# Performance work log

Measured on AMD Instinct MI355X. Metric: run time of the kernel, lower is better.

## Reference

```python
import jax, jax.numpy as jnp
import numpy as np

DIM = 512
A_HEADS = 8
C_HEADS = 4
DH = 64
EPS = 1e-5


def layer_norm(x, g, b):
    mu = jnp.mean(x, axis=-1, keepdims=True)
    var = jnp.var(x, axis=-1, keepdims=True)
    return (x - mu) * jax.lax.rsqrt(var + EPS) * g + b


def setup_inputs() -> dict:
    key = jax.random.key(0)
    ks = jax.random.split(key, 8)
    inner_a = A_HEADS * DH  # 512
    inner_c = C_HEADS * DH  # 256
    s = 0.02
    return {
        "x": jax.random.normal(ks[0], (4, 192, DIM), dtype=jnp.float32),
        # Attention branch params
        "ln1_g": jnp.ones((DIM,), jnp.float32),
        "ln1_b": jnp.zeros((DIM,), jnp.float32),
        "Wqkv": jax.random.normal(ks[1], (DIM, 3 * inner_a), jnp.float32) * s,
        "Wo": jax.random.normal(ks[2], (inner_a, DIM), jnp.float32) * s,
        "bo": jnp.zeros((DIM,), jnp.float32),
        # Trittention branch params
        "ln2_g": jnp.ones((DIM,), jnp.float32),
        "ln2_b": jnp.zeros((DIM,), jnp.float32),
        "Wabcde": jax.random.normal(ks[3], (DIM, 5 * inner_c), jnp.float32) * s,
        "babcde": jnp.zeros((5 * inner_c,), jnp.float32),
        "Wp": jax.random.normal(ks[4], (inner_c, DIM), jnp.float32) * s,
        "bp": jnp.zeros((DIM,), jnp.float32),
    }


def _attention(x, ln_g, ln_b, Wqkv, Wo, bo):
    B, T, _ = x.shape
    xn = layer_norm(x, ln_g, ln_b)
    qkv = xn @ Wqkv  # [B,T,3*H*D]
    q, k, v = jnp.split(qkv, 3, axis=-1)
    def heads(t):
        return t.reshape(B, T, A_HEADS, DH).transpose(0, 2, 1, 3)  # [B,H,T,D]
    q, k, v = heads(q), heads(k), heads(v)
    scale = DH ** -0.5
    dots = jnp.einsum('bhqd,bhkd->bhqk', q, k) * scale
    attn = jax.nn.softmax(dots, axis=-1)
    out = jnp.einsum('bhqk,bhkd->bhqd', attn, v)
    out = out.transpose(0, 2, 1, 3).reshape(B, T, A_HEADS * DH)
    return out @ Wo + bo


def _trittention(x, ln_g, ln_b, Wabcde, babcde, Wp, bp):
    B, T, _ = x.shape
    xn = layer_norm(x, ln_g, ln_b)
    proj = xn @ Wabcde + babcde  # [B,T,5*H*D]
    a, b_, c, d_, e = jnp.split(proj, 5, axis=-1)
    def heads(t):
        return t.reshape(B, T, C_HEADS, DH)  # [B,T,H,D]
    a, b_, c, d_, e = heads(a), heads(b_), heads(c), heads(d_), heads(e)
    # cubic score: [B,H,S,T,Q]
    score = jnp.einsum('bshd,bthd,bqhd->bhstq', a, b_, c) / DH
    # softmax over joint (s,t) for each query q
    score = score.transpose(0, 1, 4, 2, 3).reshape(B, C_HEADS, T, T * T)
    attn = jax.nn.softmax(score, axis=-1).reshape(B, C_HEADS, T, T, T)
    z = (jnp.einsum('bhqst,bshd->bhqd', attn, d_)
         + jnp.einsum('bhqst,bthd->bhqd', attn, e))
    z = z.transpose(0, 2, 1, 3).reshape(B, T, C_HEADS * DH)
    return z @ Wp + bp


def reference(x, ln1_g, ln1_b, Wqkv, Wo, bo, ln2_g, ln2_b, Wabcde, babcde, Wp, bp):
    return (_attention(x, ln1_g, ln1_b, Wqkv, Wo, bo)
            + _trittention(x, ln2_g, ln2_b, Wabcde, babcde, Wp, bp))
```

## Files before the change

kernel.cpp:

```cpp
#include <hip/hip_runtime.h>
#include <cstdint>


#define B_   4
#define T_   192
#define DIM_ 512
#define AH   8
#define CH   4

typedef unsigned short u16;
typedef unsigned int   u32;
typedef __attribute__((ext_vector_type(8))) short short8;
typedef __attribute__((ext_vector_type(4))) float floatx4;
typedef __attribute__((ext_vector_type(4))) int intx4;
typedef __attribute__((ext_vector_type(2))) float f32x2;
typedef __attribute__((ext_vector_type(8))) _Float16 half8;
typedef __attribute__((ext_vector_type(2))) _Float16 half2v;
typedef __attribute__((ext_vector_type(2))) __fp16 fp16x2;

union Frag  { intx4 i; short8 s; };
union FragH { intx4 i; half8 h; };

__device__ __forceinline__ floatx4 mfma16(Frag a, Frag b, floatx4 c) {
    return __builtin_amdgcn_mfma_f32_16x16x32_bf16(a.s, b.s, c, 0, 0, 0);
}
__device__ __forceinline__ floatx4 mfma16h(FragH a, FragH b, floatx4 c) {
    return __builtin_amdgcn_mfma_f32_16x16x32_f16(a.h, b.h, c, 0, 0, 0);
}

__device__ __forceinline__ float fexp2(float x) {
    return __builtin_amdgcn_exp2f(x);
}

__device__ __forceinline__ float wave_reduce_sum(float v) {
#pragma unroll
    for (int off = 32; off >= 1; off >>= 1)
        v += __shfl_xor(v, off, 64);
    return v;
}

__device__ __forceinline__ u32 pack_rne(float x, float y) {
    u32 ux = __float_as_uint(x);
    u32 uy = __float_as_uint(y);
    ux += 0x7fffu + ((ux >> 16) & 1u);
    uy += 0x7fffu + ((uy >> 16) & 1u);
    return (ux >> 16) | (uy & 0xffff0000u);
}
__device__ __forceinline__ u16 bf16_rne(float x) {
    u32 u = __float_as_uint(x);
    u += 0x7fffu + ((u >> 16) & 1u);
    return (u16)(u >> 16);
}
__device__ __forceinline__ float bf16f(u16 h) { return __uint_as_float(((u32)h) << 16); }

__device__ __forceinline__ u32 pack_f16(float x, float y) {
    union { fp16x2 h; u32 u; } cv;
    cv.h = __builtin_amdgcn_cvt_pkrtz(x, y);
    return cv.u;
}
__device__ __forceinline__ u32 mul_h2(u32 a, u32 b) {
    union { u32 u; half2v h; } ua, ub, uw;
    ua.u = a; ub.u = b;
    uw.h = ua.h * ub.h;
    return uw.u;
}

__device__ __forceinline__ Frag ld_frag8(const u16* p) {
    Frag f;
    uint2 a = *(const uint2*)p;
    uint2 b = *(const uint2*)(p + 4);
    f.i = (intx4){ (int)a.x, (int)a.y, (int)b.x, (int)b.y };
    return f;
}

#define LOG2E 1.44269504088896f

__global__ __launch_bounds__(256) void prep_kernel(
    const float* __restrict__ x,
    const float* __restrict__ g1, const float* __restrict__ b1,
    const float* __restrict__ g2, const float* __restrict__ b2,
    u16* __restrict__ x1h, u16* __restrict__ x1l,
    u16* __restrict__ x2h, u16* __restrict__ x2l,
    const float* __restrict__ Wqkv, u16* __restrict__ wqh,
    const float* __restrict__ Wab,  u16* __restrict__ wah,
    const float* __restrict__ Wo,   const float* __restrict__ Wp,
    u16* __restrict__ wofh, u16* __restrict__ wofl)
{
    __shared__ union { float t[64][65]; float red[4][2]; } u;
    const int tid = threadIdx.x;
    if (blockIdx.x < 768) {
        int row = blockIdx.x;
        const float2 v = ((const float2*)(x + (size_t)row * DIM_))[tid];
        float s  = v.x + v.y;
        float s2 = v.x * v.x + v.y * v.y;
        s  = wave_reduce_sum(s);
        s2 = wave_reduce_sum(s2);
        int w = tid >> 6;
        if ((tid & 63) == 0) { u.red[w][0] = s; u.red[w][1] = s2; }
        __syncthreads();
        float ts  = u.red[0][0] + u.red[1][0] + u.red[2][0] + u.red[3][0];
        float ts2 = u.red[0][1] + u.red[1][1] + u.red[2][1] + u.red[3][1];
        float mean = ts * (1.0f / DIM_);
        float var  = ts2 * (1.0f / DIM_) - mean * mean;
        float rstd = rsqrtf(var + 1e-5f);
        int c0 = tid * 2;
        float n0 = (v.x - mean) * rstd;
        float n1 = (v.y - mean) * rstd;
        float a0 = n0 * g1[c0] + b1[c0], a1 = n1 * g1[c0 + 1] + b1[c0 + 1];
        float c2 = n0 * g2[c0] + b2[c0], c3 = n1 * g2[c0 + 1] + b2[c0 + 1];
        u16 h0 = bf16_rne(a0), h1 = bf16_rne(a1);
        u16 h2 = bf16_rne(c2), h3 = bf16_rne(c3);
        u16 l0 = bf16_rne(a0 - bf16f(h0)), l1 = bf16_rne(a1 - bf16f(h1));
        u16 l2 = bf16_rne(c2 - bf16f(h2)), l3 = bf16_rne(c3 - bf16f(h3));
        size_t o = (size_t)row * 256 + tid;
        ((u32*)x1h)[o] = (u32)h0 | ((u32)h1 << 16);
        ((u32*)x1l)[o] = (u32)l0 | ((u32)l1 << 16);
        ((u32*)x2h)[o] = (u32)h2 | ((u32)h3 << 16);
        ((u32*)x2l)[o] = (u32)l2 | ((u32)l3 << 16);
        return;
    }
    int id = blockIdx.x - 768;
    const float* W; u16 *H, *L; int K, N, Kout, kofs, tile, wantLo;
    if (id < 192)      { W = Wqkv; H = wqh;  L = nullptr; K = 512; N = 1536; Kout = 512; kofs = 0;   tile = id;       wantLo = 0; }
    else if (id < 352) { W = Wab;  H = wah;  L = nullptr; K = 512; N = 1280; Kout = 512; kofs = 0;   tile = id - 192; wantLo = 0; }
    else if (id < 416) { W = Wo;   H = wofh; L = wofl;    K = 512; N = 512;  Kout = 768; kofs = 0;   tile = id - 352; wantLo = 1; }
    else               { W = Wp;   H = wofh; L = wofl;    K = 256; N = 512;  Kout = 768; kofs = 512; tile = id - 416; wantLo = 1; }
    int nx = N >> 6;
    int n0 = (tile % nx) * 64, k0 = (tile / nx) * 64;
    int rr = tid >> 4, c4 = (tid & 15) << 2;
#pragma unroll
    for (int p = 0; p < 4; ++p) {
        int row = rr + p * 16;
        float4 v = *(const float4*)(W + (size_t)(k0 + row) * N + n0 + c4);
        u.t[row][c4 + 0] = v.x; u.t[row][c4 + 1] = v.y;
        u.t[row][c4 + 2] = v.z; u.t[row][c4 + 3] = v.w;
    }
    __syncthreads();
#pragma unroll
    for (int p = 0; p < 4; ++p) {
        int n = rr + p * 16;
        u16 hi[4], lo[4];
#pragma unroll
        for (int c = 0; c < 4; ++c) {
            float v = u.t[c4 + c][n];
            hi[c] = bf16_rne(v);
            lo[c] = bf16_rne(v - bf16f(hi[c]));
        }
        size_t o = (size_t)(n0 + n) * Kout + kofs + k0 + c4;
        *(uint2*)&H[o] = make_uint2((u32)hi[0] | ((u32)hi[1] << 16), (u32)hi[2] | ((u32)hi[3] << 16));
        if (wantLo)
            *(uint2*)&L[o] = make_uint2((u32)lo[0] | ((u32)lo[1] << 16), (u32)lo[2] | ((u32)lo[3] << 16));
    }
}

__global__ __launch_bounds__(256) void gemm_dual(
    const u16* __restrict__ x1h, const u16* __restrict__ x1l,
    const u16* __restrict__ wqh,
    const u16* __restrict__ x2h, const u16* __restrict__ x2l,
    const u16* __restrict__ wah,
    const float* __restrict__ babcde,
    float* __restrict__ qkv, float* __restrict__ proj)
{
    __shared__ u16 As[2][64][68];
    __shared__ u16 Bs[64][68];
    const int tid = threadIdx.x;
    const int nb = blockIdx.x;
    const u16 *Ah, *Al, *BTh; const float* bias; float* C; int N, bn;
    if (nb < 24) { Ah = x1h; Al = x1l; BTh = wqh; bias = nullptr; C = qkv;  N = 1536; bn = nb * 64; }
    else         { Ah = x2h; Al = x2l; BTh = wah; bias = babcde; C = proj; N = 1280; bn = (nb - 24) * 64; }
    const int K = 512;
    const int bm = blockIdx.y * 64;
    const int lane = tid & 63, wave = tid >> 6;
    const int m16 = lane & 15, quad = lane >> 4;
    const int wm = (wave >> 1) * 32, wn = (wave & 1) * 32;
    const int r = tid >> 2, c16 = (tid & 3) * 16;

    floatx4 acc[2][2];
#pragma unroll
    for (int i = 0; i < 2; ++i)
#pragma unroll
        for (int j = 0; j < 2; ++j) acc[i][j] = (floatx4){0.f, 0.f, 0.f, 0.f};

    for (int k0 = 0; k0 < K; k0 += 64) {
        __syncthreads();
        {
            const u16* pa = Ah + (size_t)(bm + r) * K + k0 + c16;
            uint4 v0 = *(const uint4*)pa, v1 = *(const uint4*)(pa + 8);
            *(uint2*)&As[0][r][c16 + 0]  = make_uint2(v0.x, v0.y);
            *(uint2*)&As[0][r][c16 + 4]  = make_uint2(v0.z, v0.w);
            *(uint2*)&As[0][r][c16 + 8]  = make_uint2(v1.x, v1.y);
            *(uint2*)&As[0][r][c16 + 12] = make_uint2(v1.z, v1.w);
            const u16* pl = Al + (size_t)(bm + r) * K + k0 + c16;
            uint4 w0 = *(const uint4*)pl, w1 = *(const uint4*)(pl + 8);
            *(uint2*)&As[1][r][c16 + 0]  = make_uint2(w0.x, w0.y);
            *(uint2*)&As[1][r][c16 + 4]  = make_uint2(w0.z, w0.w);
            *(uint2*)&As[1][r][c16 + 8]  = make_uint2(w1.x, w1.y);
            *(uint2*)&As[1][r][c16 + 12] = make_uint2(w1.z, w1.w);
        }
        {
            const u16* pb = BTh + (size_t)(bn + r) * K + k0 + c16;
            uint4 v0 = *(const uint4*)pb, v1 = *(const uint4*)(pb + 8);
            *(uint2*)&Bs[r][c16 + 0]  = make_uint2(v0.x, v0.y);
            *(uint2*)&Bs[r][c16 + 4]  = make_uint2(v0.z, v0.w);
            *(uint2*)&Bs[r][c16 + 8]  = make_uint2(v1.x, v1.y);
            *(uint2*)&Bs[r][c16 + 12] = make_uint2(v1.z, v1.w);
        }
        __syncthreads();
#pragma unroll
        for (int ks = 0; ks < 2; ++ks) {
            const int ko = ks * 32 + quad * 8;
            Frag a0h = ld_frag8(&As[0][wm + m16][ko]);
            Frag a1h = ld_frag8(&As[0][wm + 16 + m16][ko]);
            Frag a0l = ld_frag8(&As[1][wm + m16][ko]);
            Frag a1l = ld_frag8(&As[1][wm + 16 + m16][ko]);
            Frag b0 = ld_frag8(&Bs[wn + m16][ko]);
            Frag b1 = ld_frag8(&Bs[wn + 16 + m16][ko]);
            acc[0][0] = mfma16(a0h, b0, acc[0][0]);
            acc[0][0] = mfma16(a0l, b0, acc[0][0]);
            acc[0][1] = mfma16(a0h, b1, acc[0][1]);
            acc[0][1] = mfma16(a0l, b1, acc[0][1]);
            acc[1][0] = mfma16(a1h, b0, acc[1][0]);
            acc[1][0] = mfma16(a1l, b0, acc[1][0]);
            acc[1][1] = mfma16(a1h, b1, acc[1][1]);
            acc[1][1] = mfma16(a1l, b1, acc[1][1]);
        }
    }
#pragma unroll
    for (int i = 0; i < 2; ++i)
#pragma unroll
        for (int rr = 0; rr < 4; ++rr) {
            int m = bm + wm + i * 16 + quad * 4 + rr;
#pragma unroll
            for (int j = 0; j < 2; ++j) {
                int n = bn + wn + j * 16 + m16;
                float v = acc[i][j][rr];
                if (bias) v += bias[n];
                C[(size_t)m * N + n] = v;
            }
        }
}

__global__ __launch_bounds__(256) void gemm_epilogue(
    const u16* __restrict__ aoh, const u16* __restrict__ aol,
    const u16* __restrict__ zh,  const u16* __restrict__ zl,
    const u16* __restrict__ BTh, const u16* __restrict__ BTl,
    const float* __restrict__ bo, const float* __restrict__ bp,
    float* __restrict__ C)
{
    __shared__ u16 As[2][32][68];
    __shared__ u16 Bs[2][64][68];
    const int tid = threadIdx.x;
    const int bm = blockIdx.y * 32, bn = blockIdx.x * 64;
    const int lane = tid & 63, wave = tid >> 6;
    const int m16 = lane & 15, quad = lane >> 4;
    const int wm = (wave >> 1) * 16, wn = (wave & 1) * 32;
    const int ra = tid >> 3, c8 = (tid & 7) * 8;
    const int rb = tid >> 2, c16 = (tid & 3) * 16;
    const int N = 512, K = 768;

    floatx4 acc[2];
    acc[0] = (floatx4){0.f, 0.f, 0.f, 0.f};
    acc[1] = (floatx4){0.f, 0.f, 0.f, 0.f};

    for (int k0 = 0; k0 < K; k0 += 64) {
        __syncthreads();
        const u16* pah;
        const u16* pal;
        if (k0 < 512) {
            pah = aoh + (size_t)(bm + ra) * 512 + k0 + c8;
            pal = aol + (size_t)(bm + ra) * 512 + k0 + c8;
        } else {
            pah = zh + (size_t)(bm + ra) * 256 + (k0 - 512) + c8;
            pal = zl + (size_t)(bm + ra) * 256 + (k0 - 512) + c8;
        }
        {
            uint4 v = *(const uint4*)pah;
            *(uint2*)&As[0][ra][c8 + 0] = make_uint2(v.x, v.y);
            *(uint2*)&As[0][ra][c8 + 4] = make_uint2(v.z, v.w);
            uint4 w = *(const uint4*)pal;
            *(uint2*)&As[1][ra][c8 + 0] = make_uint2(w.x, w.y);
            *(uint2*)&As[1][ra][c8 + 4] = make_uint2(w.z, w.w);
        }
        {
            const u16* pb = BTh + (size_t)(bn + rb) * K + k0 + c16;
            uint4 v0 = *(const uint4*)pb, v1 = *(const uint4*)(pb + 8);
            *(uint2*)&Bs[0][rb][c16 + 0]  = make_uint2(v0.x, v0.y);
            *(uint2*)&Bs[0][rb][c16 + 4]  = make_uint2(v0.z, v0.w);
            *(uint2*)&Bs[0][rb][c16 + 8]  = make_uint2(v1.x, v1.y);
            *(uint2*)&Bs[0][rb][c16 + 12] = make_uint2(v1.z, v1.w);
            const u16* pc = BTl + (size_t)(bn + rb) * K + k0 + c16;
            uint4 w0 = *(const uint4*)pc, w1 = *(const uint4*)(pc + 8);
            *(uint2*)&Bs[1][rb][c16 + 0]  = make_uint2(w0.x, w0.y);
            *(uint2*)&Bs[1][rb][c16 + 4]  = make_uint2(w0.z, w0.w);
            *(uint2*)&Bs[1][rb][c16 + 8]  = make_uint2(w1.x, w1.y);
            *(uint2*)&Bs[1][rb][c16 + 12] = make_uint2(w1.z, w1.w);
        }
        __syncthreads();
#pragma unroll
        for (int ks = 0; ks < 2; ++ks) {
            const int ko = ks * 32 + quad * 8;
            Frag ah = ld_frag8(&As[0][wm + m16][ko]);
            Frag al = ld_frag8(&As[1][wm + m16][ko]);
            Frag b0h = ld_frag8(&Bs[0][wn + m16][ko]);
            Frag b1h = ld_frag8(&Bs[0][wn + 16 + m16][ko]);
            Frag b0l = ld_frag8(&Bs[1][wn + m16][ko]);
            Frag b1l = ld_frag8(&Bs[1][wn + 16 + m16][ko]);
            acc[0] = mfma16(ah, b0h, acc[0]);
            acc[0] = mfma16(al, b0h, acc[0]);
            acc[0] = mfma16(ah, b0l, acc[0]);
            acc[1] = mfma16(ah, b1h, acc[1]);
            acc[1] = mfma16(al, b1h, acc[1]);
            acc[1] = mfma16(ah, b1l, acc[1]);
        }
    }
#pragma unroll
    for (int rr = 0; rr < 4; ++rr) {
        int m = bm + wm + quad * 4 + rr;
#pragma unroll
        for (int j = 0; j < 2; ++j) {
            int n = bn + wn + j * 16 + m16;
            C[(size_t)m * N + n] = acc[j][rr] + bo[n] + bp[n];
        }
    }
}

__global__ __launch_bounds__(256) void attn_mfma(
    const float* __restrict__ qkv, u16* __restrict__ aoh, u16* __restrict__ aol)
{
    __shared__ union { u16 Ks[192][68]; u16 P[32][196]; } KP;
    __shared__ union { u16 Vt[64][196]; struct { float m[2][16][68]; float r[2][16]; } mg; } VU;
    const int qt = blockIdx.x, h = blockIdx.y, b = blockIdx.z;
    const int tid = threadIdx.x;
    const int lane = tid & 63, wave = tid >> 6;
    const int m16 = lane & 15, quad = lane >> 4;
    const int qg = wave & 1;
    const int kh = wave >> 1;
    const size_t base = (size_t)(b * T_) * 1536 + h * 64;

    for (int i = tid; i < 192 * 16; i += 256) {
        int row = i >> 4, c4 = (i & 15) << 2;
        float4 kv = *(const float4*)(qkv + base + (size_t)row * 1536 + 512 + c4);
        *(uint2*)&KP.Ks[row][c4] = make_uint2(pack_rne(kv.x, kv.y), pack_rne(kv.z, kv.w));
        float4 vv = *(const float4*)(qkv + base + (size_t)row * 1536 + 1024 + c4);
        VU.Vt[c4 + 0][row] = bf16_rne(vv.x);
        VU.Vt[c4 + 1][row] = bf16_rne(vv.y);
        VU.Vt[c4 + 2][row] = bf16_rne(vv.z);
        VU.Vt[c4 + 3][row] = bf16_rne(vv.w);
    }

    Frag qf0, qf1;
    {
        const float s = 0.125f * LOG2E;
        const float* qp = qkv + base + (size_t)(qt * 32 + qg * 16 + m16) * 1536 + quad * 8;
        float4 u0 = *(const float4*)qp;
        float4 u1 = *(const float4*)(qp + 4);
        float4 u2 = *(const float4*)(qp + 32);
        float4 u3 = *(const float4*)(qp + 36);
        qf0.i = (intx4){ (int)pack_rne(u0.x * s, u0.y * s), (int)pack_rne(u0.z * s, u0.w * s),
                         (int)pack_rne(u1.x * s, u1.y * s), (int)pack_rne(u1.z * s, u1.w * s) };
        qf1.i = (intx4){ (int)pack_rne(u2.x * s, u2.y * s), (int)pack_rne(u2.z * s, u2.w * s),
                         (int)pack_rne(u3.x * s, u3.y * s), (int)pack_rne(u3.z * s, u3.w * s) };
    }
    __syncthreads();

    float ev[6][4];
    float rsum[4] = {0.f, 0.f, 0.f, 0.f};
#pragma unroll
    for (int tt = 0; tt < 6; ++tt) {
        const int krow = kh * 96 + tt * 16 + m16;
        Frag kb0 = ld_frag8(&KP.Ks[krow][quad * 8]);
        Frag kb1 = ld_frag8(&KP.Ks[krow][32 + quad * 8]);
        floatx4 accs = (floatx4){0.f, 0.f, 0.f, 0.f};
        accs = mfma16(qf0, kb0, accs);
        accs = mfma16(qf1, kb1, accs);
#pragma unroll
        for (int rr = 0; rr < 4; ++rr) {
            float e = fexp2(accs[rr]);
            ev[tt][rr] = e;
            rsum[rr] += e;
        }
    }
#pragma unroll
    for (int rr = 0; rr < 4; ++rr) {
        float v = rsum[rr];
        v += __shfl_xor(v, 1, 64);
        v += __shfl_xor(v, 2, 64);
        v += __shfl_xor(v, 4, 64);
        v += __shfl_xor(v, 8, 64);
        rsum[rr] = v;
    }

    __syncthreads();
#pragma unroll
    for (int tt = 0; tt < 6; ++tt)
#pragma unroll
        for (int rr = 0; rr < 4; ++rr)
            KP.P[qg * 16 + quad * 4 + rr][kh * 96 + tt * 16 + m16] = bf16_rne(ev[tt][rr]);

    floatx4 acco[4];
#pragma unroll
    for (int dt = 0; dt < 4; ++dt) acco[dt] = (floatx4){0.f, 0.f, 0.f, 0.f};
#pragma unroll
    for (int ts = 0; ts < 3; ++ts) {
        Frag pf = ld_frag8(&KP.P[qg * 16 + m16][kh * 96 + ts * 32 + quad * 8]);
#pragma unroll
        for (int dt = 0; dt < 4; ++dt) {
            Frag vf = ld_frag8(&VU.Vt[dt * 16 + m16][kh * 96 + ts * 32 + quad * 8]);
            acco[dt] = mfma16(pf, vf, acco[dt]);
        }
    }

    __syncthreads();
    if (kh == 1) {
#pragma unroll
        for (int dt = 0; dt < 4; ++dt)
#pragma unroll
            for (int rr = 0; rr < 4; ++rr)
                VU.mg.m[qg][quad * 4 + rr][dt * 16 + m16] = acco[dt][rr];
        if (m16 == 0) {
#pragma unroll
            for (int rr = 0; rr < 4; ++rr)
                VU.mg.r[qg][quad * 4 + rr] = rsum[rr];
        }
    }
    __syncthreads();
    if (kh == 0) {
        float rinv[4];
#pragma unroll
        for (int rr = 0; rr < 4; ++rr)
            rinv[rr] = 1.0f / (rsum[rr] + VU.mg.r[qg][quad * 4 + rr]);
#pragma unroll
        for (int dt = 0; dt < 4; ++dt)
#pragma unroll
            for (int rr = 0; rr < 4; ++rr) {
                float o = (acco[dt][rr] + VU.mg.m[qg][quad * 4 + rr][dt * 16 + m16]) * rinv[rr];
                size_t idx = (size_t)(b * T_ + qt * 32 + qg * 16 + quad * 4 + rr) * 512
                           + h * 64 + dt * 16 + m16;
                u16 hi = bf16_rne(o);
                aoh[idx] = hi;
                aol[idx] = bf16_rne(o - bf16f(hi));
            }
    }
}

__global__ __launch_bounds__(256, 3) void tritt_score_mfma(
    const float* __restrict__ proj, float* __restrict__ rs_g, float* __restrict__ rt_g)
{
    __shared__ u32 a_lds[48 * 36];
    __shared__ u32 b_lds[48 * 36];
    __shared__ float rs_lds[48][33];
    __shared__ float rt_lds[48][33];

    const int h = blockIdx.y, b = blockIdx.z;
    const int qt = blockIdx.x >> 4;
    const int sc = (blockIdx.x >> 2) & 3;
    const int tc = blockIdx.x & 3;
    const int q0 = qt * 32, s0 = sc * 48, t0 = tc * 48;
    const int tid  = threadIdx.x;
    const int lane = tid & 63, wave = tid >> 6;
    const int m16  = lane & 15, quad = lane >> 4;
    const int bh = b * CH + h;
    const size_t rowbase = (size_t)(b * T_) * 1280 + h * 64;
    const float kA = 0.015625f * LOG2E;

    for (int i = tid; i < 48 * 32; i += 256) {
        int row = i >> 5, cp = i & 31;
        const float2 va = *(const float2*)(proj + rowbase + (size_t)(s0 + row) * 1280 + 0 + cp * 2);
        a_lds[row * 36 + cp] = pack_f16(va.x * kA, va.y * kA);
        const float2 vb = *(const float2*)(proj + rowbase + (size_t)(t0 + row) * 1280 + 256 + cp * 2);
        b_lds[row * 36 + cp] = pack_f16(vb.x, vb.y);
    }

    FragH cf[2][2];
#pragma unroll
    for (int jq = 0; jq < 2; ++jq) {
        const float* cp = proj + rowbase + (size_t)(q0 + jq * 16 + m16) * 1280 + 512 + quad * 8;
        float4 u0 = *(const float4*)(cp);
        float4 u1 = *(const float4*)(cp + 4);
        float4 u2 = *(const float4*)(cp + 32);
        float4 u3 = *(const float4*)(cp + 36);
        cf[jq][0].i = (intx4){ (int)pack_f16(u0.x, u0.y), (int)pack_f16(u0.z, u0.w),
                               (int)pack_f16(u1.x, u1.y), (int)pack_f16(u1.z, u1.w) };
        cf[jq][1].i = (intx4){ (int)pack_f16(u2.x, u2.y), (int)pack_f16(u2.z, u2.w),
                               (int)pack_f16(u3.x, u3.y), (int)pack_f16(u3.z, u3.w) };
    }
    __syncthreads();

    float rt_acc[3][4][2] = {};

    for (int si = 0; si < 12; ++si) {
        const int srow = wave * 12 + si;
        const intx4 av0 = *(const intx4*)(a_lds + srow * 36 + quad * 4);
        const intx4 av1 = *(const intx4*)(a_lds + srow * 36 + 16 + quad * 4);
        float rs_s[2] = {0.f, 0.f};
#pragma unroll
        for (int tt = 0; tt < 3; ++tt) {
            const u32* bp = b_lds + (tt * 16 + m16) * 36;
            intx4 bv0 = *(const intx4*)(bp + quad * 4);
            intx4 bv1 = *(const intx4*)(bp + 16 + quad * 4);
            FragH w0, w1;
#pragma unroll
            for (int j = 0; j < 4; ++j) {
                w0.i[j] = (int)mul_h2((u32)av0[j], (u32)bv0[j]);
                w1.i[j] = (int)mul_h2((u32)av1[j], (u32)bv1[j]);
            }
#pragma unroll
            for (int jq = 0; jq < 2; ++jq) {
                floatx4 acc = (floatx4){0.f, 0.f, 0.f, 0.f};
                acc = mfma16h(w0, cf[jq][0], acc);
                acc = mfma16h(w1, cf[jq][1], acc);
#pragma unroll
                for (int rr = 0; rr < 4; ++rr) {
                    float e = fexp2(acc[rr]);
                    rt_acc[tt][rr][jq] += e;
                    rs_s[jq] += e;
                }
            }
        }
#pragma unroll
        for (int jq = 0; jq < 2; ++jq) {
            float v = rs_s[jq];
            v += __shfl_xor(v, 16, 64);
            v += __shfl_xor(v, 32, 64);
            if (lane < 16) rs_lds[srow][jq * 16 + m16] = v;
        }
    }

    __syncthreads();
    for (int w = 0; w < 4; ++w) {
        if (wave == w) {
#pragma unroll
            for (int tt = 0; tt < 3; ++tt)
#pragma unroll
                for (int rr = 0; rr < 4; ++rr) {
                    int t = tt * 16 + quad * 4 + rr;
#pragma unroll
                    for (int jq = 0; jq < 2; ++jq) {
                        if (w == 0) rt_lds[t][jq * 16 + m16] = rt_acc[tt][rr][jq];
                        else        rt_lds[t][jq * 16 + m16] += rt_acc[tt][rr][jq];
                    }
                }
        }
        __syncthreads();
    }
    for (int i = tid; i < 32 * 48; i += 256) {
        int qq = i / 48, ss = i - qq * 48;
        rs_g[((size_t)(tc * 16 + bh) * T_ + q0 + qq) * T_ + s0 + ss] = rs_lds[ss][qq];
    }
    for (int i = tid; i < 32 * 48; i += 256) {
        int qq = i / 48, t2 = i - qq * 48;
        rt_g[((size_t)(sc * 16 + bh) * T_ + q0 + qq) * T_ + t0 + t2] = rt_lds[t2][qq];
    }
}

__global__ __launch_bounds__(256) void zgemm(
    const float* __restrict__ rs_g, const float* __restrict__ rt_g,
    const float* __restrict__ proj, u16* __restrict__ zzh, u16* __restrict__ zzl)
{
    __shared__ u16 As[2][64][68];
    __shared__ u16 Bs[32][68];
    __shared__ float zred[64][4];
    __shared__ float Zl[64];
    const int mt = blockIdx.x >> 1, dh2 = blockIdx.x & 1, bh = blockIdx.y;
    const int b = bh >> 2, h = bh & 3;
    const int q0 = mt * 64;
    const int tid = threadIdx.x;
    const int lane = tid & 63, wave = tid >> 6;
    const int m16 = lane & 15, quad = lane >> 4;
    const int wm = (wave >> 1) * 32, wn = (wave & 1) * 16;
    const int r = tid >> 2, c16 = (tid & 3) * 16;

    {
        float zp = 0.f;
        const int j = tid & 3;
#pragma unroll
        for (int tc = 0; tc < 4; ++tc) {
            const float* p = rs_g + ((size_t)(tc * 16 + bh) * T_ + q0 + r) * T_ + j * 48;
#pragma unroll
            for (int s = 0; s < 48; s += 4) {
                float4 v = *(const float4*)(p + s);
                zp += (v.x + v.y) + (v.z + v.w);
            }
        }
        zred[r][j] = zp;
    }
    __syncthreads();
    if (tid < 64)
        Zl[tid] = 1.0f / (zred[tid][0] + zred[tid][1] + zred[tid][2] + zred[tid][3]);

    floatx4 acc[2];
    acc[0] = (floatx4){0.f, 0.f, 0.f, 0.f};
    acc[1] = (floatx4){0.f, 0.f, 0.f, 0.f};

    for (int k0 = 0; k0 < 384; k0 += 64) {
        __syncthreads();
        {
            float g[16];
#pragma unroll
            for (int i = 0; i < 16; ++i) g[i] = 0.f;
            if (k0 < 192) {
#pragma unroll
                for (int tc = 0; tc < 4; ++tc) {
                    const float* p = rs_g + ((size_t)(tc * 16 + bh) * T_ + q0 + r) * T_ + k0 + c16;
#pragma unroll
                    for (int i = 0; i < 16; i += 4) {
                        float4 v = *(const float4*)(p + i);
                        g[i] += v.x; g[i + 1] += v.y; g[i + 2] += v.z; g[i + 3] += v.w;
                    }
                }
            } else {
#pragma unroll
                for (int sc = 0; sc < 4; ++sc) {
                    const float* p = rt_g + ((size_t)(sc * 16 + bh) * T_ + q0 + r) * T_ + (k0 - 192) + c16;
#pragma unroll
                    for (int i = 0; i < 16; i += 4) {
                        float4 v = *(const float4*)(p + i);
                        g[i] += v.x; g[i + 1] += v.y; g[i + 2] += v.z; g[i + 3] += v.w;
                    }
                }
            }
#pragma unroll
            for (int i = 0; i < 16; ++i) {
                u16 hi = bf16_rne(g[i]);
                As[0][r][c16 + i] = hi;
                As[1][r][c16 + i] = bf16_rne(g[i] - bf16f(hi));
            }
        }
        {
            const int colbase = (k0 < 192 ? 768 : 1024) + h * 64 + dh2 * 32;
            const int s0 = (k0 < 192 ? k0 : k0 - 192);
            const int sl = tid >> 2;
            const int d4b = (tid & 3) * 4;
#pragma unroll
            for (int i = 0; i < 2; ++i) {
                int dd = d4b + i * 16;
                float4 v = *(const float4*)(proj + (size_t)(b * T_ + s0 + sl) * 1280 + colbase + dd);
                Bs[dd + 0][sl] = bf16_rne(v.x);
                Bs[dd + 1][sl] = bf16_rne(v.y);
                Bs[dd + 2][sl] = bf16_rne(v.z);
                Bs[dd + 3][sl] = bf16_rne(v.w);
            }
        }
        __syncthreads();
#pragma unroll
        for (int ks = 0; ks < 2; ++ks) {
            const int ko = ks * 32 + quad * 8;
            Frag g0h = ld_frag8(&As[0][wm + m16][ko]);
            Frag g1h = ld_frag8(&As[0][wm + 16 + m16][ko]);
            Frag g0l = ld_frag8(&As[1][wm + m16][ko]);
            Frag g1l = ld_frag8(&As[1][wm + 16 + m16][ko]);
            Frag d0 = ld_frag8(&Bs[wn + m16][ko]);
            acc[0] = mfma16(g0h, d0, acc[0]);
            acc[0] = mfma16(g0l, d0, acc[0]);
            acc[1] = mfma16(g1h, d0, acc[1]);
            acc[1] = mfma16(g1l, d0, acc[1]);
        }
    }
#pragma unroll
    for (int i = 0; i < 2; ++i)
#pragma unroll
        for (int rr = 0; rr < 4; ++rr) {
            int m = wm + i * 16 + quad * 4 + rr;
            int d = dh2 * 32 + wn + m16;
            float zv = acc[i][rr] * Zl[m];
            size_t idx = (size_t)(b * T_ + q0 + m) * 256 + h * 64 + d;
            u16 hi = bf16_rne(zv);
            zzh[idx] = hi;
            zzl[idx] = bf16_rne(zv - bf16f(hi));
        }
}

extern "C" void kernel_launch(void* const* d_in, const int* in_sizes, int n_in,
                              void* d_out, int out_size, void* d_ws, size_t ws_size,
                              hipStream_t stream)
{
    const float* x      = (const float*)d_in[0];
    const float* ln1_g  = (const float*)d_in[1];
    const float* ln1_b  = (const float*)d_in[2];
    const float* Wqkv   = (const float*)d_in[3];
    const float* Wo     = (const float*)d_in[4];
    const float* bo     = (const float*)d_in[5];
    const float* ln2_g  = (const float*)d_in[6];
    const float* ln2_b  = (const float*)d_in[7];
    const float* Wabcde = (const float*)d_in[8];
    const float* babcde = (const float*)d_in[9];
    const float* Wp     = (const float*)d_in[10];
    const float* bp     = (const float*)d_in[11];
    float* out = (float*)d_out;

    float* ws   = (float*)d_ws;
    float* proj = ws;
    u16* wofh   = (u16*)(proj + 983040);
    u16* wofl   = wofh + 393216;
    u16* aoh    = (u16*)(ws + 1376256);
    u16* aol    = aoh + 393216;
    u16* zh     = (u16*)(ws + 1769472);
    u16* zl     = zh + 196608;
    float* rs   = ws + 1966080;
    float* rt   = rs + 2359296;
    float* qkv = rs;
    u16* x1h = (u16*)(rs + 1179648);
    u16* x1l = x1h + 393216;
    u16* x2h = x1l + 393216;
    u16* x2l = x2h + 393216;
    u16* wqh = (u16*)rt;
    u16* wah = wqh + 786432;

    prep_kernel<<<1216, 256, 0, stream>>>(x, ln1_g, ln1_b, ln2_g, ln2_b,
                                          x1h, x1l, x2h, x2l,
                                          Wqkv, wqh, Wabcde, wah,
                                          Wo, Wp, wofh, wofl);
    gemm_dual<<<dim3(44, 12), 256, 0, stream>>>(x1h, x1l, wqh, x2h, x2l, wah,
                                                babcde, qkv, proj);
    attn_mfma<<<dim3(6, AH, B_), 256, 0, stream>>>(qkv, aoh, aol);
    tritt_score_mfma<<<dim3(96, CH, B_), 256, 0, stream>>>(proj, rs, rt);
    zgemm<<<dim3(6, 16), 256, 0, stream>>>(rs, rt, proj, zh, zl);
    gemm_epilogue<<<dim3(8, 24), 256, 0, stream>>>(aoh, aol, zh, zl, wofh, wofl, bo, bp, out);
}
```

Before: 167.9 us.

## Retile zgemm to 32-row by 64-column blocks and fuse normalizer sum into main loop

The zgemm kernel changes from 64-row by 32-column tiles, split across two blocks per row tile, to 32-row by 64-column tiles. Each block now covers the full head dimension, so rs/rt rows are read and summed by only one block instead of two. The separate pre-pass over rs that computed the softmax normalizer is removed; the row sum is accumulated from the values already loaded in the main loop and reduced once at the end. The grid size stays the same, but each block loads more proj columns per step.

```diff
diff --git a/kernel.cpp b/kernel.cpp
--- a/kernel.cpp
+++ b/kernel.cpp
@@ -557,37 +557,21 @@
     const float* __restrict__ rs_g, const float* __restrict__ rt_g,
     const float* __restrict__ proj, u16* __restrict__ zzh, u16* __restrict__ zzl)
 {
-    __shared__ u16 As[2][64][68];
-    __shared__ u16 Bs[32][68];
-    __shared__ float zred[64][4];
-    __shared__ float Zl[64];
-    const int mt = blockIdx.x >> 1, dh2 = blockIdx.x & 1, bh = blockIdx.y;
+    __shared__ u16 As[2][32][68];
+    __shared__ u16 Bs[64][68];
+    __shared__ float zred[32][9];
+    __shared__ float Zl[32];
+    const int mt = blockIdx.x, bh = blockIdx.y;
     const int b = bh >> 2, h = bh & 3;
-    const int q0 = mt * 64;
+    const int q0 = mt * 32;
     const int tid = threadIdx.x;
     const int lane = tid & 63, wave = tid >> 6;
     const int m16 = lane & 15, quad = lane >> 4;
-    const int wm = (wave >> 1) * 32, wn = (wave & 1) * 16;
-    const int r = tid >> 2, c16 = (tid & 3) * 16;
-
-    {
-        float zp = 0.f;
-        const int j = tid & 3;
-#pragma unroll
-        for (int tc = 0; tc < 4; ++tc) {
-            const float* p = rs_g + ((size_t)(tc * 16 + bh) * T_ + q0 + r) * T_ + j * 48;
-#pragma unroll
-            for (int s = 0; s < 48; s += 4) {
-                float4 v = *(const float4*)(p + s);
-                zp += (v.x + v.y) + (v.z + v.w);
-            }
-        }
-        zred[r][j] = zp;
-    }
-    __syncthreads();
-    if (tid < 64)
-        Zl[tid] = 1.0f / (zred[tid][0] + zred[tid][1] + zred[tid][2] + zred[tid][3]);
-
+    const int wm = (wave >> 1) * 16, wn = (wave & 1) * 32;
+    const int ra = tid >> 3, c8 = (tid & 7) * 8;
+    const int sl = tid >> 2, d4b = (tid & 3) * 4;
+
+    float zacc = 0.f;
     floatx4 acc[2];
     acc[0] = (floatx4){0.f, 0.f, 0.f, 0.f};
     acc[1] = (floatx4){0.f, 0.f, 0.f, 0.f};
@@ -595,44 +579,41 @@
     for (int k0 = 0; k0 < 384; k0 += 64) {
         __syncthreads();
         {
-            float g[16];
-#pragma unroll
-            for (int i = 0; i < 16; ++i) g[i] = 0.f;
+            float g[8];
+#pragma unroll
+            for (int i = 0; i < 8; ++i) g[i] = 0.f;
             if (k0 < 192) {
 #pragma unroll
                 for (int tc = 0; tc < 4; ++tc) {
-                    const float* p = rs_g + ((size_t)(tc * 16 + bh) * T_ + q0 + r) * T_ + k0 + c16;
-#pragma unroll
-                    for (int i = 0; i < 16; i += 4) {
-                        float4 v = *(const float4*)(p + i);
-                        g[i] += v.x; g[i + 1] += v.y; g[i + 2] += v.z; g[i + 3] += v.w;
-                    }
+                    const float* p = rs_g + ((size_t)(tc * 16 + bh) * T_ + q0 + ra) * T_ + k0 + c8;
+                    float4 v0 = *(const float4*)(p);
+                    float4 v1 = *(const float4*)(p + 4);
+                    g[0] += v0.x; g[1] += v0.y; g[2] += v0.z; g[3] += v0.w;
+                    g[4] += v1.x; g[5] += v1.y; g[6] += v1.z; g[7] += v1.w;
                 }
+                zacc += ((g[0] + g[1]) + (g[2] + g[3])) + ((g[4] + g[5]) + (g[6] + g[7]));
             } else {
 #pragma unroll
                 for (int sc = 0; sc < 4; ++sc) {
-                    const float* p = rt_g + ((size_t)(sc * 16 + bh) * T_ + q0 + r) * T_ + (k0 - 192) + c16;
-#pragma unroll
-                    for (int i = 0; i < 16; i += 4) {
-                        float4 v = *(const float4*)(p + i);
-                        g[i] += v.x; g[i + 1] += v.y; g[i + 2] += v.z; g[i + 3] += v.w;
-                    }
+                    const float* p = rt_g + ((size_t)(sc * 16 + bh) * T_ + q0 + ra) * T_ + (k0 - 192) + c8;
+                    float4 v0 = *(const float4*)(p);
+                    float4 v1 = *(const float4*)(p + 4);
+                    g[0] += v0.x; g[1] += v0.y; g[2] += v0.z; g[3] += v0.w;
+                    g[4] += v1.x; g[5] += v1.y; g[6] += v1.z; g[7] += v1.w;
                 }
             }
 #pragma unroll
-            for (int i = 0; i < 16; ++i) {
+            for (int i = 0; i < 8; ++i) {
                 u16 hi = bf16_rne(g[i]);
-                As[0][r][c16 + i] = hi;
-                As[1][r][c16 + i] = bf16_rne(g[i] - bf16f(hi));
+                As[0][ra][c8 + i] = hi;
+                As[1][ra][c8 + i] = bf16_rne(g[i] - bf16f(hi));
             }
         }
         {
-            const int colbase = (k0 < 192 ? 768 : 1024) + h * 64 + dh2 * 32;
+            const int colbase = (k0 < 192 ? 768 : 1024) + h * 64;
             const int s0 = (k0 < 192 ? k0 : k0 - 192);
-            const int sl = tid >> 2;
-            const int d4b = (tid & 3) * 4;
-#pragma unroll
-            for (int i = 0; i < 2; ++i) {
+#pragma unroll
+            for (int i = 0; i < 4; ++i) {
                 int dd = d4b + i * 16;
                 float4 v = *(const float4*)(proj + (size_t)(b * T_ + s0 + sl) * 1280 + colbase + dd);
                 Bs[dd + 0][sl] = bf16_rne(v.x);
@@ -645,24 +626,31 @@
 #pragma unroll
         for (int ks = 0; ks < 2; ++ks) {
             const int ko = ks * 32 + quad * 8;
-            Frag g0h = ld_frag8(&As[0][wm + m16][ko]);
-            Frag g1h = ld_frag8(&As[0][wm + 16 + m16][ko]);
-            Frag g0l = ld_frag8(&As[1][wm + m16][ko]);
-            Frag g1l = ld_frag8(&As[1][wm + 16 + m16][ko]);
+            Frag gh = ld_frag8(&As[0][wm + m16][ko]);
+            Frag gl = ld_frag8(&As[1][wm + m16][ko]);
             Frag d0 = ld_frag8(&Bs[wn + m16][ko]);
-            acc[0] = mfma16(g0h, d0, acc[0]);
-            acc[0] = mfma16(g0l, d0, acc[0]);
-            acc[1] = mfma16(g1h, d0, acc[1]);
-            acc[1] = mfma16(g1l, d0, acc[1]);
-        }
-    }
-#pragma unroll
-    for (int i = 0; i < 2; ++i)
+            Frag d1 = ld_frag8(&Bs[wn + 16 + m16][ko]);
+            acc[0] = mfma16(gh, d0, acc[0]);
+            acc[0] = mfma16(gl, d0, acc[0]);
+            acc[1] = mfma16(gh, d1, acc[1]);
+            acc[1] = mfma16(gl, d1, acc[1]);
+        }
+    }
+    zred[ra][tid & 7] = zacc;
+    __syncthreads();
+    if (tid < 32) {
+        float s = ((zred[tid][0] + zred[tid][1]) + (zred[tid][2] + zred[tid][3]))
+                + ((zred[tid][4] + zred[tid][5]) + (zred[tid][6] + zred[tid][7]));
+        Zl[tid] = 1.0f / s;
+    }
+    __syncthreads();
+#pragma unroll
+    for (int j = 0; j < 2; ++j)
 #pragma unroll
         for (int rr = 0; rr < 4; ++rr) {
-            int m = wm + i * 16 + quad * 4 + rr;
-            int d = dh2 * 32 + wn + m16;
-            float zv = acc[i][rr] * Zl[m];
+            int m = wm + quad * 4 + rr;
+            int d = wn + j * 16 + m16;
+            float zv = acc[j][rr] * Zl[m];
             size_t idx = (size_t)(b * T_ + q0 + m) * 256 + h * 64 + d;
             u16 hi = bf16_rne(zv);
             zzh[idx] = hi;
```

Result: faster. 159.2 us (-5.2%).
